# Performance work log

Hardware: AMD Instinct MI355X
Metric: run time of the kernel (lower is better)

The kernel has to match this reference:

```python
import jax, jax.numpy as jnp
import numpy as np


def setup_inputs() -> dict:
    key = jax.random.key(0)
    kq, kv = jax.random.split(key)
    N, To, Ti, H = 8, 1024, 4096, 512
    queries = jax.random.normal(kq, (N, To, H), dtype=jnp.float32)
    values = jax.random.normal(kv, (N, Ti, H), dtype=jnp.float32)
    return {"queries": queries, "values": values}


def reference(queries, values):
    # scores: N x To x Ti (unscaled, unmasked dot-product attention)
    scores = jnp.einsum("noh,nih->noi", queries, values)
    attn = jax.nn.softmax(scores, axis=-1)          # softmax over Ti
    out = jnp.einsum("noi,nih->noh", attn, values)  # N x To x H
    return out, attn
```

## Files before the change

### kernel.cpp

```cpp
#include <hip/hip_runtime.h>
#include <hip/hip_bf16.h>

typedef __bf16 bf16x8 __attribute__((ext_vector_type(8)));
typedef __bf16 bf16x4 __attribute__((ext_vector_type(4)));
typedef float  f32x4  __attribute__((ext_vector_type(4)));

constexpr int N_  = 8;
constexpr int TO_ = 1024;
constexpr int TI_ = 4096;
constexpr int H_  = 512;

__device__ inline void split8(const float4& x0, const float4& x1,
                              bf16x8& h, bf16x8& l)
{
    float xs[8] = {x0.x, x0.y, x0.z, x0.w, x1.x, x1.y, x1.z, x1.w};
#pragma unroll
    for (int i = 0; i < 8; ++i) {
        __bf16 hh = (__bf16)xs[i];
        h[i] = hh;
        l[i] = (__bf16)(xs[i] - (float)hh);
    }
}

__global__ __launch_bounds__(256)
void split_kernel(const float* __restrict__ X, __bf16* __restrict__ Xh,
                  __bf16* __restrict__ Xl)
{
    const size_t idx = ((size_t)blockIdx.x * 256 + threadIdx.x) * 8;
    const float4* src = reinterpret_cast<const float4*>(X + idx);
    float4 x0 = src[0], x1 = src[1];
    bf16x8 h, l;
    split8(x0, x1, h, l);
    *reinterpret_cast<bf16x8*>(Xh + idx) = h;
    *reinterpret_cast<bf16x8*>(Xl + idx) = l;
}

__global__ __launch_bounds__(256)
void vt2_kernel(const __bf16* __restrict__ Vh, __bf16* __restrict__ Vt)
{
    const int hb = blockIdx.x, tb = blockIdx.y, n = blockIdx.z;
    const int h  = hb * 64 + (threadIdx.x >> 2);
    const int tq = threadIdx.x & 3;
    const __bf16* Vn = Vh + (size_t)n * TI_ * H_;
    __bf16* Vtn = Vt + (size_t)n * H_ * TI_;

#pragma unroll
    for (int j = 0; j < 16; ++j) {
        const int t0 = tb * 512 + tq * 128 + j * 8;
        bf16x8 o;
#pragma unroll
        for (int e = 0; e < 8; ++e)
            o[e] = Vn[(size_t)(t0 + e) * H_ + h];
        *reinterpret_cast<bf16x8*>(&Vtn[(size_t)h * TI_ + t0]) = o;
    }
}

__global__ __launch_bounds__(256, 2)
void qk3_kernel(const __bf16* __restrict__ Qh, const __bf16* __restrict__ Ql,
                const __bf16* __restrict__ Vh, const __bf16* __restrict__ Vl,
                float* __restrict__ S)
{
    __shared__ __bf16 Ah[128 * 64];
    __shared__ __bf16 Al[128 * 64];
    __shared__ __bf16 Bh[128 * 64];
    __shared__ __bf16 Bl[128 * 64];

    const int tt = blockIdx.x, mt = blockIdx.y, n = blockIdx.z;
    const size_t qoff = ((size_t)n * TO_ + (size_t)mt * 128) * H_;
    const size_t voff = ((size_t)n * TI_ + (size_t)tt * 128) * H_;
    const __bf16* Qhb = Qh + qoff;
    const __bf16* Qlb = Ql + qoff;
    const __bf16* Vhb = Vh + voff;
    const __bf16* Vlb = Vl + voff;

    const int tid  = threadIdx.x;
    const int lane = tid & 63, wave = tid >> 6;
    const int wr = wave >> 1, wc = wave & 1;
    const int fr = lane & 15, fq = lane >> 4;

    const int srow = tid >> 3;
    const int sc   = tid & 7;

    auto stage = [&](const __bf16* __restrict__ g, __bf16* lds, int k0) {
#pragma unroll
        for (int i = 0; i < 4; ++i) {
            const int row = i * 32 + srow;
            const int csw = sc ^ (row & 7);
            const __bf16* gs = g + (size_t)row * H_ + k0 + csw * 8;
            const int q0 = (i * 256 + wave * 64) * 16;
            __builtin_amdgcn_global_load_lds(
                (const __attribute__((address_space(1))) void*)gs,
                (__attribute__((address_space(3))) void*)((char*)lds + q0),
                16, 0, 0);
        }
    };

    f32x4 acc[4][4] = {};

    for (int kt = 0; kt < H_ / 64; ++kt) {
        const int k0 = kt * 64;
        __syncthreads();
        stage(Qhb, Ah, k0);
        stage(Qlb, Al, k0);
        stage(Vhb, Bh, k0);
        stage(Vlb, Bl, k0);
        __syncthreads();

#pragma unroll
        for (int kk = 0; kk < 2; ++kk) {
            bf16x8 ah[4], al[4], bh[4], bl[4];
#pragma unroll
            for (int m = 0; m < 4; ++m) {
                const int row = wr * 64 + m * 16 + fr;
                const int cs  = (kk * 4 + fq) ^ (row & 7);
                ah[m] = *reinterpret_cast<const bf16x8*>(&Ah[row * 64 + cs * 8]);
                al[m] = *reinterpret_cast<const bf16x8*>(&Al[row * 64 + cs * 8]);
            }
#pragma unroll
            for (int j = 0; j < 4; ++j) {
                const int row = wc * 64 + j * 16 + fr;
                const int cs  = (kk * 4 + fq) ^ (row & 7);
                bh[j] = *reinterpret_cast<const bf16x8*>(&Bh[row * 64 + cs * 8]);
                bl[j] = *reinterpret_cast<const bf16x8*>(&Bl[row * 64 + cs * 8]);
            }
#pragma unroll
            for (int m = 0; m < 4; ++m)
#pragma unroll
                for (int j = 0; j < 4; ++j) {
                    acc[m][j] = __builtin_amdgcn_mfma_f32_16x16x32_bf16(ah[m], bh[j], acc[m][j], 0, 0, 0);
                    acc[m][j] = __builtin_amdgcn_mfma_f32_16x16x32_bf16(ah[m], bl[j], acc[m][j], 0, 0, 0);
                    acc[m][j] = __builtin_amdgcn_mfma_f32_16x16x32_bf16(al[m], bh[j], acc[m][j], 0, 0, 0);
                }
        }
    }

    float* Sb = S + ((size_t)n * TO_ + (size_t)mt * 128) * TI_ + (size_t)tt * 128;
    const int crow0 = wr * 64 + fq * 4;
    const int ccol0 = wc * 64 + fr;
#pragma unroll
    for (int m = 0; m < 4; ++m)
#pragma unroll
        for (int j = 0; j < 4; ++j)
#pragma unroll
            for (int r = 0; r < 4; ++r)
                Sb[(size_t)(crow0 + m * 16 + r) * TI_ + (ccol0 + j * 16)] = acc[m][j][r];
}

__global__ __launch_bounds__(256)
void softmax2_kernel(float* __restrict__ S, __bf16* __restrict__ A16)
{
    const int wave = threadIdx.x >> 6, lane = threadIdx.x & 63;
    const size_t row = (size_t)blockIdx.x * 4 + wave;
    float4* p = reinterpret_cast<float4*>(S + row * TI_);
    __bf16* p16 = A16 + row * TI_;

    float4 v[16];
    float m = -3.0e38f;
#pragma unroll
    for (int j = 0; j < 16; ++j) {
        v[j] = p[j * 64 + lane];
        m = fmaxf(m, fmaxf(fmaxf(v[j].x, v[j].y), fmaxf(v[j].z, v[j].w)));
    }
#pragma unroll
    for (int s = 32; s > 0; s >>= 1) m = fmaxf(m, __shfl_xor(m, s));

    constexpr float L2E = 1.4426950408889634f;
    float sum = 0.f;
#pragma unroll
    for (int j = 0; j < 16; ++j) {
        v[j].x = exp2f((v[j].x - m) * L2E);
        v[j].y = exp2f((v[j].y - m) * L2E);
        v[j].z = exp2f((v[j].z - m) * L2E);
        v[j].w = exp2f((v[j].w - m) * L2E);
        sum += (v[j].x + v[j].y) + (v[j].z + v[j].w);
    }
#pragma unroll
    for (int s = 32; s > 0; s >>= 1) sum += __shfl_xor(sum, s);

    const float inv = 1.0f / sum;
#pragma unroll
    for (int j = 0; j < 16; ++j) {
        v[j].x *= inv; v[j].y *= inv; v[j].z *= inv; v[j].w *= inv;
        p[j * 64 + lane] = v[j];
        bf16x4 o;
        o[0] = (__bf16)v[j].x; o[1] = (__bf16)v[j].y;
        o[2] = (__bf16)v[j].z; o[3] = (__bf16)v[j].w;
        *reinterpret_cast<bf16x4*>(&p16[(j * 64 + lane) * 4]) = o;
    }
}

__global__ __launch_bounds__(512, 2)
void pv7_kernel(const __bf16* __restrict__ A16, const __bf16* __restrict__ Vt,
                float* __restrict__ O, float* __restrict__ P)
{
    __shared__ __bf16 AsmA[128 * 64], AsmB[128 * 64];
    __shared__ __bf16 BsmA[256 * 64], BsmB[256 * 64];

    const int flat = blockIdx.x;
    const int mt = flat >> 5;
    const int g  = flat & 31;
    const int n  = g >> 2;
    const int ht = (g >> 1) & 1;
    const int kc = g & 1;

    const __bf16* Ab = A16 + ((size_t)n * TO_ + (size_t)mt * 128) * TI_ + (size_t)kc * 2048;
    const __bf16* Bb = Vt  + ((size_t)n * H_  + (size_t)ht * 256) * TI_ + (size_t)kc * 2048;

    const int tid = threadIdx.x, lane = tid & 63, wave = tid >> 6;
    const int wm = wave >> 2, wh = wave & 3;
    const int fr = lane & 15, fq = lane >> 4;

    auto stage = [&](__bf16* asm_, __bf16* bsm_, int k0) {
#pragma unroll
        for (int i = 0; i < 2; ++i) {
            const int q   = i * 512 + tid;
            const int row = q >> 3, c = q & 7;
            const int csw = c ^ (row & 7);
            const __bf16* gs = Ab + (size_t)row * TI_ + k0 + csw * 8;
            const int q0 = (i * 512 + wave * 64) * 16;
            __builtin_amdgcn_global_load_lds(
                (const __attribute__((address_space(1))) void*)gs,
                (__attribute__((address_space(3))) void*)((char*)asm_ + q0),
                16, 0, 0);
        }
#pragma unroll
        for (int i = 0; i < 4; ++i) {
            const int q   = i * 512 + tid;
            const int row = q >> 3, c = q & 7;
            const int csw = c ^ (row & 7);
            const __bf16* gs = Bb + (size_t)row * TI_ + k0 + csw * 8;
            const int q0 = (i * 512 + wave * 64) * 16;
            __builtin_amdgcn_global_load_lds(
                (const __attribute__((address_space(1))) void*)gs,
                (__attribute__((address_space(3))) void*)((char*)bsm_ + q0),
                16, 0, 0);
        }
    };

    f32x4 acc[4][4] = {};

    auto compute = [&](const __bf16* Asm, const __bf16* Bsm) {
#pragma unroll
        for (int kk = 0; kk < 2; ++kk) {
            bf16x8 a[4], b[4];
#pragma unroll
            for (int m = 0; m < 4; ++m) {
                const int row = wm * 64 + m * 16 + fr;
                const int cs  = (kk * 4 + fq) ^ (row & 7);
                a[m] = *reinterpret_cast<const bf16x8*>(&Asm[row * 64 + cs * 8]);
            }
#pragma unroll
            for (int j = 0; j < 4; ++j) {
                const int row = wh * 64 + j * 16 + fr;
                const int cs  = (kk * 4 + fq) ^ (row & 7);
                b[j] = *reinterpret_cast<const bf16x8*>(&Bsm[row * 64 + cs * 8]);
            }
#pragma unroll
            for (int m = 0; m < 4; ++m)
#pragma unroll
                for (int j = 0; j < 4; ++j)
                    acc[m][j] = __builtin_amdgcn_mfma_f32_16x16x32_bf16(
                        a[m], b[j], acc[m][j], 0, 0, 0);
        }
    };

    constexpr int NT = 2048 / 64;
    stage(AsmA, BsmA, 0);
    __syncthreads();
    for (int kt = 0; kt < NT; kt += 2) {
        if (kt + 1 < NT) stage(AsmB, BsmB, (kt + 1) * 64);
        compute(AsmA, BsmA);
        __syncthreads();
        if (kt + 2 < NT) stage(AsmA, BsmA, (kt + 2) * 64);
        compute(AsmB, BsmB);
        __syncthreads();
    }

    float* D  = (kc == 0) ? O : P;
    float* Db = D + ((size_t)n * TO_ + (size_t)mt * 128) * H_ + ht * 256;
#pragma unroll
    for (int m = 0; m < 4; ++m) {
        const int orow = wm * 64 + m * 16 + fq * 4;
#pragma unroll
        for (int j = 0; j < 4; ++j) {
            const int ocol = wh * 64 + j * 16 + fr;
#pragma unroll
            for (int r = 0; r < 4; ++r)
                Db[(size_t)(orow + r) * H_ + ocol] = acc[m][j][r];
        }
    }
}

__global__ __launch_bounds__(256)
void add_kernel(float4* __restrict__ o, const float4* __restrict__ p)
{
    const size_t i = (size_t)blockIdx.x * 256 + threadIdx.x;
    float4 a = o[i], b = p[i];
    a.x += b.x; a.y += b.y; a.z += b.z; a.w += b.w;
    o[i] = a;
}

constexpr int BM1 = 128, BN1 = 128, BK1 = 32, LP1 = BK1 + 8;

__global__ __launch_bounds__(256, 2)
void qk_kernel(const float* __restrict__ Q, const float* __restrict__ V,
               float* __restrict__ S)
{
    __shared__ __bf16 Ah[BM1 * LP1];
    __shared__ __bf16 Al[BM1 * LP1];
    __shared__ __bf16 Bh[BN1 * LP1];
    __shared__ __bf16 Bl[BN1 * LP1];

    const int tt = blockIdx.x, mt = blockIdx.y, n = blockIdx.z;
    const float* Qb = Q + ((size_t)n * TO_ + (size_t)mt * BM1) * H_;
    const float* Vb = V + ((size_t)n * TI_ + (size_t)tt * BN1) * H_;

    const int tid  = threadIdx.x;
    const int lane = tid & 63, wave = tid >> 6;
    const int wr = wave >> 1, wc = wave & 1;
    const int srow = tid >> 2, scg = tid & 3;

    f32x4 acc[4][4] = {};

    for (int k0 = 0; k0 < H_; k0 += BK1) {
        __syncthreads();
#pragma unroll
        for (int half = 0; half < 2; ++half) {
            const int r = srow + half * 64;
            {
                const float4* src =
                    reinterpret_cast<const float4*>(Qb + (size_t)r * H_ + k0 + scg * 8);
                float4 x0 = src[0], x1 = src[1];
                bf16x8 hv, lv;
                split8(x0, x1, hv, lv);
                *reinterpret_cast<bf16x8*>(&Ah[r * LP1 + scg * 8]) = hv;
                *reinterpret_cast<bf16x8*>(&Al[r * LP1 + scg * 8]) = lv;
            }
            {
                const float4* src =
                    reinterpret_cast<const float4*>(Vb + (size_t)r * H_ + k0 + scg * 8);
                float4 x0 = src[0], x1 = src[1];
                bf16x8 hv, lv;
                split8(x0, x1, hv, lv);
                *reinterpret_cast<bf16x8*>(&Bh[r * LP1 + scg * 8]) = hv;
                *reinterpret_cast<bf16x8*>(&Bl[r * LP1 + scg * 8]) = lv;
            }
        }
        __syncthreads();

        bf16x8 ah[4], al[4], bh[4], bl[4];
        const int fr = lane & 15, fg = (lane >> 4) * 8;
#pragma unroll
        for (int m = 0; m < 4; ++m) {
            const int row = wr * 64 + m * 16 + fr;
            ah[m] = *reinterpret_cast<const bf16x8*>(&Ah[row * LP1 + fg]);
            al[m] = *reinterpret_cast<const bf16x8*>(&Al[row * LP1 + fg]);
        }
#pragma unroll
        for (int j = 0; j < 4; ++j) {
            const int row = wc * 64 + j * 16 + fr;
            bh[j] = *reinterpret_cast<const bf16x8*>(&Bh[row * LP1 + fg]);
            bl[j] = *reinterpret_cast<const bf16x8*>(&Bl[row * LP1 + fg]);
        }
#pragma unroll
        for (int m = 0; m < 4; ++m)
#pragma unroll
            for (int j = 0; j < 4; ++j) {
                acc[m][j] = __builtin_amdgcn_mfma_f32_16x16x32_bf16(ah[m], bh[j], acc[m][j], 0, 0, 0);
                acc[m][j] = __builtin_amdgcn_mfma_f32_16x16x32_bf16(ah[m], bl[j], acc[m][j], 0, 0, 0);
                acc[m][j] = __builtin_amdgcn_mfma_f32_16x16x32_bf16(al[m], bh[j], acc[m][j], 0, 0, 0);
            }
    }

    float* Sb = S + ((size_t)n * TO_ + (size_t)mt * BM1) * TI_ + (size_t)tt * BN1;
    const int crow0 = wr * 64 + (lane >> 4) * 4;
    const int ccol0 = wc * 64 + (lane & 15);
#pragma unroll
    for (int m = 0; m < 4; ++m)
#pragma unroll
        for (int j = 0; j < 4; ++j)
#pragma unroll
            for (int r = 0; r < 4; ++r)
                Sb[(size_t)(crow0 + m * 16 + r) * TI_ + (ccol0 + j * 16)] = acc[m][j][r];
}

__global__ __launch_bounds__(256)
void softmax_kernel(float* __restrict__ S)
{
    const int wave = threadIdx.x >> 6, lane = threadIdx.x & 63;
    const size_t row = (size_t)blockIdx.x * 4 + wave;
    float4* p = reinterpret_cast<float4*>(S + row * TI_);

    float4 v[16];
    float m = -3.0e38f;
#pragma unroll
    for (int j = 0; j < 16; ++j) {
        v[j] = p[j * 64 + lane];
        m = fmaxf(m, fmaxf(fmaxf(v[j].x, v[j].y), fmaxf(v[j].z, v[j].w)));
    }
#pragma unroll
    for (int s = 32; s > 0; s >>= 1) m = fmaxf(m, __shfl_xor(m, s));

    constexpr float L2E = 1.4426950408889634f;
    float sum = 0.f;
#pragma unroll
    for (int j = 0; j < 16; ++j) {
        v[j].x = exp2f((v[j].x - m) * L2E);
        v[j].y = exp2f((v[j].y - m) * L2E);
        v[j].z = exp2f((v[j].z - m) * L2E);
        v[j].w = exp2f((v[j].w - m) * L2E);
        sum += (v[j].x + v[j].y) + (v[j].z + v[j].w);
    }
#pragma unroll
    for (int s = 32; s > 0; s >>= 1) sum += __shfl_xor(sum, s);

    const float inv = 1.0f / sum;
#pragma unroll
    for (int j = 0; j < 16; ++j) {
        v[j].x *= inv; v[j].y *= inv; v[j].z *= inv; v[j].w *= inv;
        p[j * 64 + lane] = v[j];
    }
}

__global__ __launch_bounds__(256)
void vt_kernel(const float* __restrict__ V, __bf16* __restrict__ Vt)
{
    const int hb = blockIdx.x, tb = blockIdx.y, n = blockIdx.z;
    const int h  = hb * 64 + (threadIdx.x >> 2);
    const int tq = threadIdx.x & 3;
    const float* Vn = V + (size_t)n * TI_ * H_;
    __bf16* Vtn = Vt + (size_t)n * H_ * TI_;

#pragma unroll
    for (int j = 0; j < 16; ++j) {
        const int t0 = tb * 512 + tq * 128 + j * 8;
        bf16x8 o;
#pragma unroll
        for (int e = 0; e < 8; ++e)
            o[e] = (__bf16)Vn[(size_t)(t0 + e) * H_ + h];
        *reinterpret_cast<bf16x8*>(&Vtn[(size_t)h * TI_ + t0]) = o;
    }
}

constexpr int PBM = 32, PBK = 64, PLP = PBK + 8;

__global__ __launch_bounds__(512, 2)
void pv_fast_kernel(const float* __restrict__ A, const __bf16* __restrict__ Vt,
                    float* __restrict__ O)
{
    __shared__ __bf16 AsmF[PBM * PLP];
    __shared__ __bf16 BsmF[512 * PLP];

    const int n = blockIdx.x, mt = blockIdx.y;
    const float*  Ab = A  + ((size_t)n * TO_ + (size_t)mt * PBM) * TI_;
    const __bf16* Vb = Vt + (size_t)n * H_ * TI_;

    const int tid = threadIdx.x, lane = tid & 63, wv = tid >> 6;
    const int ar = tid >> 4;
    const int ac = (tid & 15) * 4;
    const int bh = tid >> 3;
    const int bc = (tid & 7) * 8;

    float4 aReg;
    bf16x8 bReg[8];

    auto loadTile = [&](int k0) {
        aReg = *reinterpret_cast<const float4*>(Ab + (size_t)ar * TI_ + k0 + ac);
#pragma unroll
        for (int i = 0; i < 8; ++i)
            bReg[i] = *reinterpret_cast<const bf16x8*>(
                Vb + (size_t)(bh + i * 64) * TI_ + k0 + bc);
    };

    f32x4 acc[2][4] = {};
    const int fr = lane & 15, fg = (lane >> 4) * 8;

    loadTile(0);
    constexpr int NT = TI_ / PBK;
    for (int kt = 0; kt < NT; ++kt) {
        __syncthreads();
        {
            bf16x4 av;
            av[0] = (__bf16)aReg.x; av[1] = (__bf16)aReg.y;
            av[2] = (__bf16)aReg.z; av[3] = (__bf16)aReg.w;
            *reinterpret_cast<bf16x4*>(&AsmF[ar * PLP + ac]) = av;
#pragma unroll
            for (int i = 0; i < 8; ++i)
                *reinterpret_cast<bf16x8*>(&BsmF[(bh + i * 64) * PLP + bc]) = bReg[i];
        }
        __syncthreads();
        if (kt + 1 < NT) loadTile((kt + 1) * PBK);

#pragma unroll
        for (int kk = 0; kk < 2; ++kk) {
            bf16x8 af[2], bfr[4];
#pragma unroll
            for (int m = 0; m < 2; ++m)
                af[m] = *reinterpret_cast<const bf16x8*>(
                    &AsmF[(m * 16 + fr) * PLP + kk * 32 + fg]);
#pragma unroll
            for (int j = 0; j < 4; ++j)
                bfr[j] = *reinterpret_cast<const bf16x8*>(
                    &BsmF[(wv * 64 + j * 16 + fr) * PLP + kk * 32 + fg]);
#pragma unroll
            for (int m = 0; m < 2; ++m)
#pragma unroll
                for (int j = 0; j < 4; ++j)
                    acc[m][j] = __builtin_amdgcn_mfma_f32_16x16x32_bf16(
                        af[m], bfr[j], acc[m][j], 0, 0, 0);
        }
    }

    float* Ob = O + ((size_t)n * TO_ + (size_t)mt * PBM) * H_ + wv * 64;
    const int crow = (lane >> 4) * 4;
    const int ccol = lane & 15;
#pragma unroll
    for (int m = 0; m < 2; ++m)
#pragma unroll
        for (int j = 0; j < 4; ++j)
#pragma unroll
            for (int r = 0; r < 4; ++r)
                Ob[(size_t)(m * 16 + crow + r) * H_ + j * 16 + ccol] = acc[m][j][r];
}

extern "C" void kernel_launch(void* const* d_in, const int* in_sizes, int n_in,
                              void* d_out, int out_size, void* d_ws, size_t ws_size,
                              hipStream_t stream)
{
    const float* Q = (const float*)d_in[0];
    const float* V = (const float*)d_in[1];
    float* out  = (float*)d_out;
    float* attn = out + (size_t)N_ * TO_ * H_;

    const size_t NV = (size_t)N_ * TI_ * H_;
    const size_t NQ = (size_t)N_ * TO_ * H_;
    const size_t FULL_BYTES = (3 * NV + 2 * NQ) * sizeof(__bf16);
    const size_t VT_BYTES   = NV * sizeof(__bf16);

    __bf16* wsb = (__bf16*)d_ws;
    __bf16* Vt = wsb;
    __bf16* Vh = wsb + NV;
    __bf16* Vl = wsb + 2 * NV;
    __bf16* Qh = wsb + 3 * NV;
    __bf16* Ql = wsb + 3 * NV + NQ;
    __bf16* A16 = wsb + NV;
    float*  Ppart = (float*)(wsb + 3 * NV);

    if (ws_size >= FULL_BYTES) {
        split_kernel<<<dim3(NV / (256 * 8)), 256, 0, stream>>>(V, Vh, Vl);
        split_kernel<<<dim3(NQ / (256 * 8)), 256, 0, stream>>>(Q, Qh, Ql);
        vt2_kernel<<<dim3(H_ / 64, TI_ / 512, N_), 256, 0, stream>>>(Vh, Vt);
        qk3_kernel<<<dim3(TI_ / 128, TO_ / 128, N_), 256, 0, stream>>>(Qh, Ql, Vh, Vl, attn);
        softmax2_kernel<<<dim3(N_ * TO_ / 4), 256, 0, stream>>>(attn, A16);
        pv7_kernel<<<dim3(256), 512, 0, stream>>>(A16, Vt, out, Ppart);
        add_kernel<<<dim3((unsigned)(NQ / 4 / 256)), 256, 0, stream>>>(
            (float4*)out, (const float4*)Ppart);
    } else if (ws_size >= VT_BYTES) {
        vt_kernel<<<dim3(H_ / 64, TI_ / 512, N_), 256, 0, stream>>>(V, Vt);
        qk_kernel<<<dim3(TI_ / BN1, TO_ / BM1, N_), 256, 0, stream>>>(Q, V, attn);
        softmax_kernel<<<dim3(N_ * TO_ / 4), 256, 0, stream>>>(attn);
        pv_fast_kernel<<<dim3(N_, TO_ / PBM), 512, 0, stream>>>(attn, Vt, out);
    }
}
```

Baseline: 250.5 us.

## Fuse V split with transpose and halve QK k-tile for higher occupancy

Merges the V hi/lo split and the Vh transpose into one kernel that transposes through a shared-memory tile. This removes the separate transpose pass, which re-read Vh with strided gathers. The QK kernel now uses a 32-wide k-tile with a new swizzle, cutting LDS use in half so launch bounds can allow 4 blocks per CU. The cost is twice as many k-iterations and barriers for the same work.

Result: slower. 259.0 us (+3.4%).

```diff
diff --git a/kernel.cpp b/kernel.cpp
--- a/kernel.cpp
+++ b/kernel.cpp
@@ -36,34 +36,61 @@
 }
 
 __global__ __launch_bounds__(256)
-void vt2_kernel(const __bf16* __restrict__ Vh, __bf16* __restrict__ Vt)
-{
-    const int hb = blockIdx.x, tb = blockIdx.y, n = blockIdx.z;
-    const int h  = hb * 64 + (threadIdx.x >> 2);
+void splitv2_kernel(const float* __restrict__ V, __bf16* __restrict__ Vh,
+                    __bf16* __restrict__ Vl, __bf16* __restrict__ Vt)
+{
+    __shared__ __bf16 Lh[64][72];
+
+    const int tt = blockIdx.x, hb = blockIdx.y, n = blockIdx.z;
+    const int t0 = tt * 64, h0 = hb * 64;
+    const float* Vn = V + (size_t)n * TI_ * H_;
+    __bf16* Vhn = Vh + (size_t)n * TI_ * H_;
+    __bf16* Vln = Vl + (size_t)n * TI_ * H_;
+    __bf16* Vtn = Vt + (size_t)n * H_ * TI_;
+
+    const int tr = threadIdx.x >> 4;
+    const int hc = (threadIdx.x & 15) * 4;
+
+#pragma unroll
+    for (int j = 0; j < 4; ++j) {
+        const int t = tr + j * 16;
+        const size_t o = (size_t)(t0 + t) * H_ + h0 + hc;
+        float4 x = *reinterpret_cast<const float4*>(Vn + o);
+        bf16x4 hv, lv;
+        float xs[4] = {x.x, x.y, x.z, x.w};
+#pragma unroll
+        for (int e = 0; e < 4; ++e) {
+            __bf16 hh = (__bf16)xs[e];
+            hv[e] = hh;
+            lv[e] = (__bf16)(xs[e] - (float)hh);
+        }
+        *reinterpret_cast<bf16x4*>(Vhn + o) = hv;
+        *reinterpret_cast<bf16x4*>(Vln + o) = lv;
+        *reinterpret_cast<bf16x4*>(&Lh[t][hc]) = hv;
+    }
+    __syncthreads();
+
+    const int th = threadIdx.x >> 2;
     const int tq = threadIdx.x & 3;
-    const __bf16* Vn = Vh + (size_t)n * TI_ * H_;
-    __bf16* Vtn = Vt + (size_t)n * H_ * TI_;
-
-#pragma unroll
-    for (int j = 0; j < 16; ++j) {
-        const int t0 = tb * 512 + tq * 128 + j * 8;
+#pragma unroll
+    for (int s = 0; s < 2; ++s) {
+        const int tb = tq * 16 + s * 8;
         bf16x8 o;
 #pragma unroll
-        for (int e = 0; e < 8; ++e)
-            o[e] = Vn[(size_t)(t0 + e) * H_ + h];
-        *reinterpret_cast<bf16x8*>(&Vtn[(size_t)h * TI_ + t0]) = o;
-    }
-}
-
-__global__ __launch_bounds__(256, 2)
-void qk3_kernel(const __bf16* __restrict__ Qh, const __bf16* __restrict__ Ql,
-                const __bf16* __restrict__ Vh, const __bf16* __restrict__ Vl,
-                float* __restrict__ S)
-{
-    __shared__ __bf16 Ah[128 * 64];
-    __shared__ __bf16 Al[128 * 64];
-    __shared__ __bf16 Bh[128 * 64];
-    __shared__ __bf16 Bl[128 * 64];
+        for (int e = 0; e < 8; ++e) o[e] = Lh[tb + e][th];
+        *reinterpret_cast<bf16x8*>(&Vtn[(size_t)(h0 + th) * TI_ + t0 + tb]) = o;
+    }
+}
+
+__global__ __launch_bounds__(256, 4)
+void qk3b_kernel(const __bf16* __restrict__ Qh, const __bf16* __restrict__ Ql,
+                 const __bf16* __restrict__ Vh, const __bf16* __restrict__ Vl,
+                 float* __restrict__ S)
+{
+    __shared__ __bf16 Ah[128 * 32];
+    __shared__ __bf16 Al[128 * 32];
+    __shared__ __bf16 Bh[128 * 32];
+    __shared__ __bf16 Bl[128 * 32];
 
     const int tt = blockIdx.x, mt = blockIdx.y, n = blockIdx.z;
     const size_t qoff = ((size_t)n * TO_ + (size_t)mt * 128) * H_;
@@ -78,15 +105,16 @@
     const int wr = wave >> 1, wc = wave & 1;
     const int fr = lane & 15, fq = lane >> 4;
 
-    const int srow = tid >> 3;
-    const int sc   = tid & 7;
-
     auto stage = [&](const __bf16* __restrict__ g, __bf16* lds, int k0) {
 #pragma unroll
-        for (int i = 0; i < 4; ++i) {
-            const int row = i * 32 + srow;
-            const int csw = sc ^ (row & 7);
-            const __bf16* gs = g + (size_t)row * H_ + k0 + csw * 8;
+        for (int i = 0; i < 2; ++i) {
+            const int q  = i * 256 + tid;
+            const int p  = q >> 3;
+            const int sp = q & 7;
+            const int s  = sp ^ (p & 7);
+            const int row = p * 2 + (s >> 2);
+            const int c   = s & 3;
+            const __bf16* gs = g + (size_t)row * H_ + k0 + c * 8;
             const int q0 = (i * 256 + wave * 64) * 16;
             __builtin_amdgcn_global_load_lds(
                 (const __attribute__((address_space(1))) void*)gs,
@@ -95,10 +123,17 @@
         }
     };
 
+    auto faddr = [&](const __bf16* lds, int row) -> const bf16x8* {
+        const int p  = row >> 1;
+        const int s  = ((row & 1) << 2) | fq;
+        const int sp = s ^ (p & 7);
+        return reinterpret_cast<const bf16x8*>((const char*)lds + p * 128 + sp * 16);
+    };
+
     f32x4 acc[4][4] = {};
 
-    for (int kt = 0; kt < H_ / 64; ++kt) {
-        const int k0 = kt * 64;
+    for (int kt = 0; kt < H_ / 32; ++kt) {
+        const int k0 = kt * 32;
         __syncthreads();
         stage(Qhb, Ah, k0);
         stage(Qlb, Al, k0);
@@ -106,32 +141,27 @@
         stage(Vlb, Bl, k0);
         __syncthreads();
 
-#pragma unroll
-        for (int kk = 0; kk < 2; ++kk) {
-            bf16x8 ah[4], al[4], bh[4], bl[4];
-#pragma unroll
-            for (int m = 0; m < 4; ++m) {
-                const int row = wr * 64 + m * 16 + fr;
-                const int cs  = (kk * 4 + fq) ^ (row & 7);
-                ah[m] = *reinterpret_cast<const bf16x8*>(&Ah[row * 64 + cs * 8]);
-                al[m] = *reinterpret_cast<const bf16x8*>(&Al[row * 64 + cs * 8]);
+        bf16x8 ah[4], al[4], bh[4], bl[4];
+#pragma unroll
+        for (int m = 0; m < 4; ++m) {
+            const int row = wr * 64 + m * 16 + fr;
+            ah[m] = *faddr(Ah, row);
+            al[m] = *faddr(Al, row);
+        }
+#pragma unroll
+        for (int j = 0; j < 4; ++j) {
+            const int row = wc * 64 + j * 16 + fr;
+            bh[j] = *faddr(Bh, row);
+            bl[j] = *faddr(Bl, row);
+        }
+#pragma unroll
+        for (int m = 0; m < 4; ++m)
+#pragma unroll
+            for (int j = 0; j < 4; ++j) {
+                acc[m][j] = __builtin_amdgcn_mfma_f32_16x16x32_bf16(ah[m], bh[j], acc[m][j], 0, 0, 0);
+                acc[m][j] = __builtin_amdgcn_mfma_f32_16x16x32_bf16(ah[m], bl[j], acc[m][j], 0, 0, 0);
+                acc[m][j] = __builtin_amdgcn_mfma_f32_16x16x32_bf16(al[m], bh[j], acc[m][j], 0, 0, 0);
             }
-#pragma unroll
-            for (int j = 0; j < 4; ++j) {
-                const int row = wc * 64 + j * 16 + fr;
-                const int cs  = (kk * 4 + fq) ^ (row & 7);
-                bh[j] = *reinterpret_cast<const bf16x8*>(&Bh[row * 64 + cs * 8]);
-                bl[j] = *reinterpret_cast<const bf16x8*>(&Bl[row * 64 + cs * 8]);
-            }
-#pragma unroll
-            for (int m = 0; m < 4; ++m)
-#pragma unroll
-                for (int j = 0; j < 4; ++j) {
-                    acc[m][j] = __builtin_amdgcn_mfma_f32_16x16x32_bf16(ah[m], bh[j], acc[m][j], 0, 0, 0);
-                    acc[m][j] = __builtin_amdgcn_mfma_f32_16x16x32_bf16(ah[m], bl[j], acc[m][j], 0, 0, 0);
-                    acc[m][j] = __builtin_amdgcn_mfma_f32_16x16x32_bf16(al[m], bh[j], acc[m][j], 0, 0, 0);
-                }
-        }
     }
 
     float* Sb = S + ((size_t)n * TO_ + (size_t)mt * 128) * TI_ + (size_t)tt * 128;
@@ -547,10 +577,9 @@
     float*  Ppart = (float*)(wsb + 3 * NV);
 
     if (ws_size >= FULL_BYTES) {
-        split_kernel<<<dim3(NV / (256 * 8)), 256, 0, stream>>>(V, Vh, Vl);
+        splitv2_kernel<<<dim3(TI_ / 64, H_ / 64, N_), 256, 0, stream>>>(V, Vh, Vl, Vt);
         split_kernel<<<dim3(NQ / (256 * 8)), 256, 0, stream>>>(Q, Qh, Ql);
-        vt2_kernel<<<dim3(H_ / 64, TI_ / 512, N_), 256, 0, stream>>>(Vh, Vt);
-        qk3_kernel<<<dim3(TI_ / 128, TO_ / 128, N_), 256, 0, stream>>>(Qh, Ql, Vh, Vl, attn);
+        qk3b_kernel<<<dim3(TI_ / 128, TO_ / 128, N_), 256, 0, stream>>>(Qh, Ql, Vh, Vl, attn);
         softmax2_kernel<<<dim3(N_ * TO_ / 4), 256, 0, stream>>>(attn, A16);
         pv7_kernel<<<dim3(256), 512, 0, stream>>>(A16, Vt, out, Ppart);
         add_kernel<<<dim3((unsigned)(NQ / 4 / 256)), 256, 0, stream>>>(
```
